# Kernel tuning notes

Hardware: AMD Instinct MI355X
Metric: run time of the kernel (lower is better)

The kernel has to match this reference:

```python
import jax, jax.numpy as jnp
import numpy as np

N = 1024
DH = 64   # XH feature dim (<= DOUT)
DP = 32   # XP feature dim
DIN = 64  # input_dim (== output_dim, required by f_psi applied to vij)
DOUT = 64 # output_dim
BN_EPS = 1e-5
SIGMA = 0.1


def setup_inputs() -> dict:
    key = jax.random.key(0)
    ks = jax.random.split(key, 8)
    return {
        "XH": jax.random.normal(ks[0], (N, DH), dtype=jnp.float32),
        "XP": jax.random.normal(ks[1], (N, DP), dtype=jnp.float32),
        "XX": jax.random.normal(ks[2], (N, DIN), dtype=jnp.float32),
        "K": 16,
        # nn.Parameter weight/bias: normal(0, 0.01)
        "weight": 0.01 * jax.random.normal(ks[3], (DIN, DOUT), dtype=jnp.float32),
        "bias": 0.01 * jax.random.normal(ks[4], (DOUT,), dtype=jnp.float32),
        # f_psi Linear params (torch kaiming-uniform ~ small uniform)
        "psi_w": jax.random.uniform(ks[5], (DOUT, DIN), dtype=jnp.float32, minval=-1.0, maxval=1.0) / np.sqrt(DIN),
        "psi_b": jax.random.uniform(ks[6], (DOUT,), dtype=jnp.float32, minval=-1.0, maxval=1.0) / np.sqrt(DIN),
        # BatchNorm1d affine params
        "gamma": jnp.ones((DOUT,), dtype=jnp.float32),
        "beta": jnp.zeros((DOUT,), dtype=jnp.float32),
    }


def _pairwise_norm(X):
    # [N, N] matrix of L2 norms of row differences (as in torch.norm(X[:,None]-X, dim=2))
    return jnp.linalg.norm(X[:, None, :] - X[None, :, :], axis=2)


def _adjacency(XH, XP, K, sigma=SIGMA):
    eps = float(np.finfo(np.float64).eps)
    XHs = XH / (sigma + eps)
    WHo = _pairwise_norm(XHs)
    WH = jnp.exp(-((WHo - WHo.min()) / (WHo.max() - WHo.min())) / 2)
    Wlo = _pairwise_norm(XP)
    Wl = jnp.exp(-((Wlo - Wlo.min()) / (Wlo.max() - Wlo.min())))
    WW = WH + 0.2 * Wl
    _, idx = jax.lax.top_k(WW, K)                       # per-row top-K neighbors
    n = WW.shape[0]
    mask = jnp.zeros_like(WW).at[jnp.arange(n)[:, None], idx].set(1.0)
    mask = mask + mask.T                                # symmetrize
    # Original sets Adj=WW/WW=1 where mask!=0 and Adj=WW-WW=0 elsewhere -> binary adjacency
    return (mask > 0).astype(WW.dtype)


def reference(XH, XP, XX, K, weight, bias, psi_w, psi_b, gamma, beta):
    Adj = _adjacency(XH, XP, K)                         # [N, N], {0,1}
    x = XX @ weight                                     # [N, D]
    vi = x[None, :, :] * Adj[:, :, None]                # [N, N, D]: vi[i,j] = x[j]*Adj[i,j]
    vij = x[None, :, :] + vi                            # [N, N, D]
    # f_psi: Linear -> BatchNorm1d (training-mode batch stats) -> Sigmoid, over N*N rows
    h = jnp.einsum('ijd,ed->ije', vij, psi_w) + psi_b   # [N, N, D]
    mu = h.mean(axis=(0, 1))                            # [D]
    var = h.var(axis=(0, 1))                            # biased var, as torch BN
    att = jax.nn.sigmoid((h - mu) * jax.lax.rsqrt(var + BN_EPS) * gamma + beta)
    # self-loop attention forced to 1 on the diagonal
    eye = jnp.eye(x.shape[0], dtype=bool)[:, :, None]
    att = jnp.where(eye, jnp.float32(1.0), att)
    out = (att * vi).sum(axis=0) + bias                 # [N, D]
    return (out[:, :XH.shape[1]], XP, out)
```

## Files before the change

### kernel.cpp

```cpp
#include <hip/hip_runtime.h>
#include <cfloat>

#define NN 1024


__global__ __launch_bounds__(256) void gcn_prep(const float* __restrict__ XH,
                                                const float* __restrict__ XP,
                                                const float* __restrict__ XX,
                                                const float* __restrict__ W,
                                                const float* __restrict__ psi_w,
                                                const int* __restrict__ kptr,
                                                float* __restrict__ XHT,
                                                float* __restrict__ XPT,
                                                float* __restrict__ x,
                                                float* __restrict__ y,
                                                double* __restrict__ Sbins,
                                                int* __restrict__ cdeg) {
    const int b = blockIdx.x;
    const int tid = threadIdx.x;
    __shared__ float th[64][65];
    __shared__ float tp[32][65];
    __shared__ float xybuf[4][2][64];
    if (b < 16) {
        const int j0 = b * 64;
#pragma unroll
        for (int it = 0; it < 16; ++it) {
            int idx = it * 256 + tid;
            int jl = idx >> 6, d = idx & 63;
            th[d][jl] = XH[(j0 + jl) * 64 + d];
        }
#pragma unroll
        for (int it = 0; it < 8; ++it) {
            int idx = it * 256 + tid;
            int jl = idx >> 5, d = idx & 31;
            tp[d][jl] = XP[(j0 + jl) * 32 + d];
        }
        __syncthreads();
#pragma unroll
        for (int it = 0; it < 16; ++it) {
            int idx = it * 256 + tid;
            int d = idx >> 6, jl = idx & 63;
            XHT[d * NN + j0 + jl] = th[d][jl];
        }
#pragma unroll
        for (int it = 0; it < 8; ++it) {
            int idx = it * 256 + tid;
            int d = idx >> 6, jl = idx & 63;
            XPT[d * NN + j0 + jl] = tp[d][jl];
        }
    } else if (b < 80) {
        const int w = tid >> 6, e = tid & 63;
        const int ibase = (b - 16) * 16 + w * 4;
#pragma unroll
        for (int r = 0; r < 4; ++r) {
            const int i = ibase + r;
            xybuf[w][0][e] = XX[i * 64 + e];
            __syncthreads();
            float acc = 0.f;
#pragma unroll
            for (int d = 0; d < 64; ++d) acc += xybuf[w][0][d] * W[d * 64 + e];
            x[i * 64 + e] = acc;
            xybuf[w][1][e] = acc;
            __syncthreads();
            float acc2 = 0.f;
            const float* pw = psi_w + e * 64;
#pragma unroll
            for (int d = 0; d < 64; ++d) acc2 += xybuf[w][1][d] * pw[d];
            y[i * 64 + e] = acc2;
        }
    } else {
        const int K = *kptr;
#pragma unroll
        for (int k = 0; k < 16; ++k) Sbins[tid * 16 + k] = 0.0;
#pragma unroll
        for (int q = 0; q < 4; ++q) cdeg[q * 256 + tid] = K;
    }
}

__global__ __launch_bounds__(256) void gcn_dist(const float* __restrict__ XH,
                                                const float* __restrict__ XP,
                                                const float* __restrict__ XHT,
                                                const float* __restrict__ XPT,
                                                float* __restrict__ dhp,
                                                float* __restrict__ dpp,
                                                float2* __restrict__ bmax) {
    const int b = blockIdx.x;
    const int i0 = (b >> 2) * 4;
    const int j = (b & 3) * 256 + threadIdx.x;
    const int tid = threadIdx.x;
    __shared__ float shi[4][64];
    __shared__ float spi[4][32];
    shi[tid >> 6][tid & 63] = XH[(i0 + (tid >> 6)) * 64 + (tid & 63)];
    if (tid < 128) spi[tid >> 5][tid & 31] = XP[(i0 + (tid >> 5)) * 32 + (tid & 31)];
    __syncthreads();
    float dh[4] = {0.f, 0.f, 0.f, 0.f}, dp[4] = {0.f, 0.f, 0.f, 0.f};
#pragma unroll 16
    for (int d = 0; d < 64; ++d) {
        float v = XHT[d * NN + j];
#pragma unroll
        for (int r = 0; r < 4; ++r) { float t = v - shi[r][d]; dh[r] += t * t; }
    }
#pragma unroll 16
    for (int d = 0; d < 32; ++d) {
        float v = XPT[d * NN + j];
#pragma unroll
        for (int r = 0; r < 4; ++r) { float t = v - spi[r][d]; dp[r] += t * t; }
    }
#pragma unroll
    for (int r = 0; r < 4; ++r) {
        dhp[(size_t)(i0 + r) * NN + j] = sqrtf(dh[r]);
        dpp[(size_t)(i0 + r) * NN + j] = sqrtf(dp[r]);
    }
    float mh = fmaxf(fmaxf(dh[0], dh[1]), fmaxf(dh[2], dh[3]));
    float mp = fmaxf(fmaxf(dp[0], dp[1]), fmaxf(dp[2], dp[3]));
#pragma unroll
    for (int m = 1; m < 64; m <<= 1) {
        mh = fmaxf(mh, __shfl_xor(mh, m));
        mp = fmaxf(mp, __shfl_xor(mp, m));
    }
    __shared__ float wmx[4][2];
    if ((tid & 63) == 0) { wmx[tid >> 6][0] = mh; wmx[tid >> 6][1] = mp; }
    __syncthreads();
    if (tid == 0) {
        float a = fmaxf(fmaxf(wmx[0][0], wmx[1][0]), fmaxf(wmx[2][0], wmx[3][0]));
        float b2 = fmaxf(fmaxf(wmx[0][1], wmx[1][1]), fmaxf(wmx[2][1], wmx[3][1]));
        bmax[b] = make_float2(a, b2);
    }
}

__global__ __launch_bounds__(256) void gcn_topk(const float* __restrict__ dhp,
                                                const float* __restrict__ dpp,
                                                const float2* __restrict__ bmax,
                                                const int* __restrict__ kptr,
                                                int* __restrict__ eidx,
                                                int* __restrict__ cdeg) {
    const int tid = threadIdx.x;
    const int w = tid >> 6, lane = tid & 63;
    const int i = blockIdx.x * 4 + w;
    float mh = 0.f, mp = 0.f;
#pragma unroll
    for (int q = 0; q < 4; ++q) {
        float2 v = bmax[q * 256 + tid];
        mh = fmaxf(mh, v.x); mp = fmaxf(mp, v.y);
    }
#pragma unroll
    for (int m = 1; m < 64; m <<= 1) {
        mh = fmaxf(mh, __shfl_xor(mh, m));
        mp = fmaxf(mp, __shfl_xor(mp, m));
    }
    __shared__ float warr[4][2];
    if (lane == 0) { warr[w][0] = mh; warr[w][1] = mp; }
    __syncthreads();
    mh = fmaxf(fmaxf(warr[0][0], warr[1][0]), fmaxf(warr[2][0], warr[3][0]));
    mp = fmaxf(fmaxf(warr[0][1], warr[1][1]), fmaxf(warr[2][1], warr[3][1]));
    const float cH = -0.5f / sqrtf(mh);
    const float cP = -1.0f / sqrtf(mp);
    const float4* dh4 = (const float4*)(dhp + (size_t)i * NN);
    const float4* dp4 = (const float4*)(dpp + (size_t)i * NN);
    unsigned long long kk[16];
#pragma unroll
    for (int s = 0; s < 4; ++s) {
        float4 a = dh4[s * 64 + lane];
        float4 b = dp4[s * 64 + lane];
        float w0 = __expf(a.x * cH) + 0.2f * __expf(b.x * cP);
        float w1 = __expf(a.y * cH) + 0.2f * __expf(b.y * cP);
        float w2 = __expf(a.z * cH) + 0.2f * __expf(b.z * cP);
        float w3 = __expf(a.w * cH) + 0.2f * __expf(b.w * cP);
        int jb = s * 256 + lane * 4;
        kk[s * 4 + 0] = ((unsigned long long)__float_as_uint(w0) << 32) | (unsigned)(1023 - (jb + 0));
        kk[s * 4 + 1] = ((unsigned long long)__float_as_uint(w1) << 32) | (unsigned)(1023 - (jb + 1));
        kk[s * 4 + 2] = ((unsigned long long)__float_as_uint(w2) << 32) | (unsigned)(1023 - (jb + 2));
        kk[s * 4 + 3] = ((unsigned long long)__float_as_uint(w3) << 32) | (unsigned)(1023 - (jb + 3));
    }
    const int K = *kptr;
    int jsave = 0;
    for (int t = 0; t < K; ++t) {
        unsigned long long bk = 0ull;
#pragma unroll
        for (int v = 0; v < 16; ++v) bk = kk[v] > bk ? kk[v] : bk;
#pragma unroll
        for (int m = 1; m < 64; m <<= 1) {
            unsigned long long o = __shfl_xor(bk, m);
            bk = o > bk ? o : bk;
        }
        int j = 1023 - (int)(bk & 0x3FFull);
        if (lane == t) jsave = j;
        if (((j >> 2) & 63) == lane) {
            int slot = ((j >> 8) << 2) | (j & 3);
#pragma unroll
            for (int v = 0; v < 16; ++v)
                if (v == slot) kk[v] = 0ull;
        }
    }
    if (lane < K) {
        eidx[i * 16 + lane] = jsave;
        atomicAdd(&cdeg[jsave], 1);
    }
}

__global__ __launch_bounds__(256) void gcn_overlap(const int* __restrict__ eidx,
                                                   int* __restrict__ cdeg) {
    const int gid = blockIdx.x * 256 + threadIdx.x;
    const int i = gid >> 4;
    const int j = eidx[gid];
    if (j < 0) return;
    const int4* ej = (const int4*)(eidx + j * 16);
    bool rec = false;
#pragma unroll
    for (int q = 0; q < 4; ++q) {
        int4 e = ej[q];
        rec |= (e.x == i) | (e.y == i) | (e.z == i) | (e.w == i);
    }
    if (rec) atomicSub(&cdeg[j], 1);
}

__global__ __launch_bounds__(256) void gcn_stats(const float* __restrict__ y,
                                                 const int* __restrict__ cdeg,
                                                 double* __restrict__ S1,
                                                 double* __restrict__ S2) {
    const int w = threadIdx.x >> 6, e = threadIdx.x & 63;
    const int j = blockIdx.x * 4 + w;
    const int c = cdeg[j];
    const double yd = (double)y[j * 64 + e];
    const int bin = (j & 31) * 64 + e;
    atomicAdd(&S1[bin], (double)(NN + c) * yd);
    atomicAdd(&S2[bin], (double)(NN + 3 * c) * yd * yd);
}

__global__ __launch_bounds__(256) void gcn_out(const float* __restrict__ x,
                                               const float* __restrict__ y,
                                               const int* __restrict__ cdeg,
                                               const float* __restrict__ gamma,
                                               const float* __restrict__ beta,
                                               const double* __restrict__ S1,
                                               const double* __restrict__ S2,
                                               const float* __restrict__ bias,
                                               const float* __restrict__ XP,
                                               float* __restrict__ out) {
    const int w = threadIdx.x >> 6, e = threadIdx.x & 63;
    const int j = blockIdx.x * 4 + w;
    double s1 = 0.0, s2 = 0.0;
#pragma unroll
    for (int b = 0; b < 32; ++b) { s1 += S1[b * 64 + e]; s2 += S2[b * 64 + e]; }
    const double m = s1 / 1048576.0;
    const double var = s2 / 1048576.0 - m * m;
    const float m0e = (float)m;
    const float scalee = (float)(1.0 / sqrt(var + 1e-5)) * gamma[e];
    float t = y[j * 64 + e];
    float z = (2.f * t - m0e) * scalee + beta[e];
    float s = 1.f / (1.f + expf(-z));
    float val = x[j * 64 + e] * ((float)(cdeg[j] - 1) * s + 1.f) + bias[e];
    out[j * 64 + e] = val;
    out[98304 + j * 64 + e] = val;
    if (e < 32) out[65536 + j * 32 + e] = XP[j * 32 + e];
}

extern "C" void kernel_launch(void* const* d_in, const int* in_sizes, int n_in,
                              void* d_out, int out_size, void* d_ws, size_t ws_size,
                              hipStream_t stream) {
    const float* XH    = (const float*)d_in[0];
    const float* XP    = (const float*)d_in[1];
    const float* XX    = (const float*)d_in[2];
    const int*   Kp    = (const int*)d_in[3];
    const float* W     = (const float*)d_in[4];
    const float* bias  = (const float*)d_in[5];
    const float* psi_w = (const float*)d_in[6];
    const float* psi_b = (const float*)d_in[7];
    const float* gamma = (const float*)d_in[8];
    const float* beta  = (const float*)d_in[9];
    (void)psi_b;
    float* out = (float*)d_out;
    char* ws = (char*)d_ws;

    float* dhp   = (float*)ws;
    float* dpp   = (float*)(ws + 0x400000);
    float* XHT   = (float*)(ws + 0x800000);
    float* XPT   = (float*)(ws + 0x840000);
    int* eidx    = (int*)(ws + 0x860000);
    float2* bmax = (float2*)(ws + 0x870000);
    int* cdeg    = (int*)(ws + 0x872000);
    double* S1   = (double*)(ws + 0x874000);
    double* S2   = (double*)(ws + 0x878000);
    float* x     = (float*)(ws + 0x880000);
    float* y     = (float*)(ws + 0x8C0000);

    gcn_prep<<<dim3(81), dim3(256), 0, stream>>>(XH, XP, XX, W, psi_w, Kp, XHT, XPT, x, y, S1, cdeg);
    gcn_dist<<<dim3(1024), dim3(256), 0, stream>>>(XH, XP, XHT, XPT, dhp, dpp, bmax);
    gcn_topk<<<dim3(256), dim3(256), 0, stream>>>(dhp, dpp, bmax, Kp, eidx, cdeg);
    gcn_overlap<<<dim3(64), dim3(256), 0, stream>>>(eidx, cdeg);
    gcn_stats<<<dim3(256), dim3(256), 0, stream>>>(y, cdeg, S1, S2);
    gcn_out<<<dim3(256), dim3(256), 0, stream>>>(x, y, cdeg, gamma, beta, S1, S2, bias, XP, out);
}
```

Measured before the change: 147.1 us.

## Fuse all stages into one cooperative kernel with grid-wide syncs

Replaces six separate kernel launches with a single cooperative launch of 256 blocks that uses grid.sync() between the prep, distance, top-k, overlap, stats and output stages. The distance stage is remapped so each block covers four rows across all 1024 columns instead of launching 1024 blocks. The aim is to remove per-launch overhead and inter-kernel gaps. In exchange, parallelism in the distance stage drops to 256 blocks, and each grid barrier has its own cost.

```diff
diff --git a/kernel.cpp b/kernel.cpp
--- a/kernel.cpp
+++ b/kernel.cpp
@@ -1,26 +1,37 @@
 #include <hip/hip_runtime.h>
+#include <hip/hip_cooperative_groups.h>
 #include <cfloat>
 
+namespace cg = cooperative_groups;
+
 #define NN 1024
 
 
-__global__ __launch_bounds__(256) void gcn_prep(const float* __restrict__ XH,
-                                                const float* __restrict__ XP,
-                                                const float* __restrict__ XX,
-                                                const float* __restrict__ W,
-                                                const float* __restrict__ psi_w,
-                                                const int* __restrict__ kptr,
-                                                float* __restrict__ XHT,
-                                                float* __restrict__ XPT,
-                                                float* __restrict__ x,
-                                                float* __restrict__ y,
-                                                double* __restrict__ Sbins,
-                                                int* __restrict__ cdeg) {
+__global__ __launch_bounds__(256, 1) void gcn_mega(
+    const float* __restrict__ XH, const float* __restrict__ XP,
+    const float* __restrict__ XX, const int* __restrict__ kptr,
+    const float* __restrict__ W, const float* __restrict__ bias,
+    const float* __restrict__ psi_w, const float* __restrict__ gamma,
+    const float* __restrict__ beta,
+    float* __restrict__ dhp, float* __restrict__ dpp,
+    float* __restrict__ XHT, float* __restrict__ XPT,
+    int* __restrict__ eidx, float2* __restrict__ bmax,
+    int* __restrict__ cdeg, double* __restrict__ S1, double* __restrict__ S2,
+    float* __restrict__ x, float* __restrict__ y,
+    float* __restrict__ out)
+{
+    cg::grid_group grid = cg::this_grid();
     const int b = blockIdx.x;
     const int tid = threadIdx.x;
+    const int w = tid >> 6, lane = tid & 63;
+
     __shared__ float th[64][65];
     __shared__ float tp[32][65];
     __shared__ float xybuf[4][2][64];
+    __shared__ float shi[4][64];
+    __shared__ float spi[4][32];
+    __shared__ float wred[4][2];
+
     if (b < 16) {
         const int j0 = b * 64;
 #pragma unroll
@@ -49,210 +60,182 @@
             XPT[d * NN + j0 + jl] = tp[d][jl];
         }
     } else if (b < 80) {
-        const int w = tid >> 6, e = tid & 63;
         const int ibase = (b - 16) * 16 + w * 4;
 #pragma unroll
         for (int r = 0; r < 4; ++r) {
             const int i = ibase + r;
-            xybuf[w][0][e] = XX[i * 64 + e];
+            xybuf[w][0][lane] = XX[i * 64 + lane];
             __syncthreads();
             float acc = 0.f;
 #pragma unroll
-            for (int d = 0; d < 64; ++d) acc += xybuf[w][0][d] * W[d * 64 + e];
-            x[i * 64 + e] = acc;
-            xybuf[w][1][e] = acc;
+            for (int d = 0; d < 64; ++d) acc += xybuf[w][0][d] * W[d * 64 + lane];
+            x[i * 64 + lane] = acc;
+            xybuf[w][1][lane] = acc;
             __syncthreads();
             float acc2 = 0.f;
-            const float* pw = psi_w + e * 64;
+            const float* pw = psi_w + lane * 64;
 #pragma unroll
             for (int d = 0; d < 64; ++d) acc2 += xybuf[w][1][d] * pw[d];
-            y[i * 64 + e] = acc2;
-        }
-    } else {
+            y[i * 64 + lane] = acc2;
+        }
+    } else if (b == 80) {
         const int K = *kptr;
 #pragma unroll
-        for (int k = 0; k < 16; ++k) Sbins[tid * 16 + k] = 0.0;
+        for (int k = 0; k < 16; ++k) S1[tid * 16 + k] = 0.0;
 #pragma unroll
         for (int q = 0; q < 4; ++q) cdeg[q * 256 + tid] = K;
     }
-}
-
-__global__ __launch_bounds__(256) void gcn_dist(const float* __restrict__ XH,
-                                                const float* __restrict__ XP,
-                                                const float* __restrict__ XHT,
-                                                const float* __restrict__ XPT,
-                                                float* __restrict__ dhp,
-                                                float* __restrict__ dpp,
-                                                float2* __restrict__ bmax) {
-    const int b = blockIdx.x;
-    const int i0 = (b >> 2) * 4;
-    const int j = (b & 3) * 256 + threadIdx.x;
-    const int tid = threadIdx.x;
-    __shared__ float shi[4][64];
-    __shared__ float spi[4][32];
-    shi[tid >> 6][tid & 63] = XH[(i0 + (tid >> 6)) * 64 + (tid & 63)];
-    if (tid < 128) spi[tid >> 5][tid & 31] = XP[(i0 + (tid >> 5)) * 32 + (tid & 31)];
-    __syncthreads();
-    float dh[4] = {0.f, 0.f, 0.f, 0.f}, dp[4] = {0.f, 0.f, 0.f, 0.f};
+    grid.sync();
+
+    {
+        const int i0 = b * 4;
+        shi[w][lane] = XH[(i0 + w) * 64 + lane];
+        if (tid < 128) spi[tid >> 5][tid & 31] = XP[(i0 + (tid >> 5)) * 32 + (tid & 31)];
+        __syncthreads();
+        float mh = 0.f, mp = 0.f;
+#pragma unroll
+        for (int jc = 0; jc < 4; ++jc) {
+            const int j = jc * 256 + tid;
+            float dh[4] = {0.f, 0.f, 0.f, 0.f}, dp[4] = {0.f, 0.f, 0.f, 0.f};
 #pragma unroll 16
-    for (int d = 0; d < 64; ++d) {
-        float v = XHT[d * NN + j];
-#pragma unroll
-        for (int r = 0; r < 4; ++r) { float t = v - shi[r][d]; dh[r] += t * t; }
-    }
+            for (int d = 0; d < 64; ++d) {
+                float v = XHT[d * NN + j];
+#pragma unroll
+                for (int r = 0; r < 4; ++r) { float t = v - shi[r][d]; dh[r] += t * t; }
+            }
 #pragma unroll 16
-    for (int d = 0; d < 32; ++d) {
-        float v = XPT[d * NN + j];
-#pragma unroll
-        for (int r = 0; r < 4; ++r) { float t = v - spi[r][d]; dp[r] += t * t; }
-    }
-#pragma unroll
-    for (int r = 0; r < 4; ++r) {
-        dhp[(size_t)(i0 + r) * NN + j] = sqrtf(dh[r]);
-        dpp[(size_t)(i0 + r) * NN + j] = sqrtf(dp[r]);
-    }
-    float mh = fmaxf(fmaxf(dh[0], dh[1]), fmaxf(dh[2], dh[3]));
-    float mp = fmaxf(fmaxf(dp[0], dp[1]), fmaxf(dp[2], dp[3]));
-#pragma unroll
-    for (int m = 1; m < 64; m <<= 1) {
-        mh = fmaxf(mh, __shfl_xor(mh, m));
-        mp = fmaxf(mp, __shfl_xor(mp, m));
-    }
-    __shared__ float wmx[4][2];
-    if ((tid & 63) == 0) { wmx[tid >> 6][0] = mh; wmx[tid >> 6][1] = mp; }
-    __syncthreads();
-    if (tid == 0) {
-        float a = fmaxf(fmaxf(wmx[0][0], wmx[1][0]), fmaxf(wmx[2][0], wmx[3][0]));
-        float b2 = fmaxf(fmaxf(wmx[0][1], wmx[1][1]), fmaxf(wmx[2][1], wmx[3][1]));
-        bmax[b] = make_float2(a, b2);
-    }
-}
-
-__global__ __launch_bounds__(256) void gcn_topk(const float* __restrict__ dhp,
-                                                const float* __restrict__ dpp,
-                                                const float2* __restrict__ bmax,
-                                                const int* __restrict__ kptr,
-                                                int* __restrict__ eidx,
-                                                int* __restrict__ cdeg) {
-    const int tid = threadIdx.x;
-    const int w = tid >> 6, lane = tid & 63;
-    const int i = blockIdx.x * 4 + w;
-    float mh = 0.f, mp = 0.f;
-#pragma unroll
-    for (int q = 0; q < 4; ++q) {
-        float2 v = bmax[q * 256 + tid];
-        mh = fmaxf(mh, v.x); mp = fmaxf(mp, v.y);
-    }
-#pragma unroll
-    for (int m = 1; m < 64; m <<= 1) {
-        mh = fmaxf(mh, __shfl_xor(mh, m));
-        mp = fmaxf(mp, __shfl_xor(mp, m));
-    }
-    __shared__ float warr[4][2];
-    if (lane == 0) { warr[w][0] = mh; warr[w][1] = mp; }
-    __syncthreads();
-    mh = fmaxf(fmaxf(warr[0][0], warr[1][0]), fmaxf(warr[2][0], warr[3][0]));
-    mp = fmaxf(fmaxf(warr[0][1], warr[1][1]), fmaxf(warr[2][1], warr[3][1]));
-    const float cH = -0.5f / sqrtf(mh);
-    const float cP = -1.0f / sqrtf(mp);
-    const float4* dh4 = (const float4*)(dhp + (size_t)i * NN);
-    const float4* dp4 = (const float4*)(dpp + (size_t)i * NN);
-    unsigned long long kk[16];
-#pragma unroll
-    for (int s = 0; s < 4; ++s) {
-        float4 a = dh4[s * 64 + lane];
-        float4 b = dp4[s * 64 + lane];
-        float w0 = __expf(a.x * cH) + 0.2f * __expf(b.x * cP);
-        float w1 = __expf(a.y * cH) + 0.2f * __expf(b.y * cP);
-        float w2 = __expf(a.z * cH) + 0.2f * __expf(b.z * cP);
-        float w3 = __expf(a.w * cH) + 0.2f * __expf(b.w * cP);
-        int jb = s * 256 + lane * 4;
-        kk[s * 4 + 0] = ((unsigned long long)__float_as_uint(w0) << 32) | (unsigned)(1023 - (jb + 0));
-        kk[s * 4 + 1] = ((unsigned long long)__float_as_uint(w1) << 32) | (unsigned)(1023 - (jb + 1));
-        kk[s * 4 + 2] = ((unsigned long long)__float_as_uint(w2) << 32) | (unsigned)(1023 - (jb + 2));
-        kk[s * 4 + 3] = ((unsigned long long)__float_as_uint(w3) << 32) | (unsigned)(1023 - (jb + 3));
-    }
-    const int K = *kptr;
-    int jsave = 0;
-    for (int t = 0; t < K; ++t) {
-        unsigned long long bk = 0ull;
-#pragma unroll
-        for (int v = 0; v < 16; ++v) bk = kk[v] > bk ? kk[v] : bk;
+            for (int d = 0; d < 32; ++d) {
+                float v = XPT[d * NN + j];
+#pragma unroll
+                for (int r = 0; r < 4; ++r) { float t = v - spi[r][d]; dp[r] += t * t; }
+            }
+#pragma unroll
+            for (int r = 0; r < 4; ++r) {
+                dhp[(size_t)(i0 + r) * NN + j] = sqrtf(dh[r]);
+                dpp[(size_t)(i0 + r) * NN + j] = sqrtf(dp[r]);
+            }
+            mh = fmaxf(mh, fmaxf(fmaxf(dh[0], dh[1]), fmaxf(dh[2], dh[3])));
+            mp = fmaxf(mp, fmaxf(fmaxf(dp[0], dp[1]), fmaxf(dp[2], dp[3])));
+        }
 #pragma unroll
         for (int m = 1; m < 64; m <<= 1) {
-            unsigned long long o = __shfl_xor(bk, m);
-            bk = o > bk ? o : bk;
-        }
-        int j = 1023 - (int)(bk & 0x3FFull);
-        if (lane == t) jsave = j;
-        if (((j >> 2) & 63) == lane) {
-            int slot = ((j >> 8) << 2) | (j & 3);
-#pragma unroll
-            for (int v = 0; v < 16; ++v)
-                if (v == slot) kk[v] = 0ull;
-        }
-    }
-    if (lane < K) {
-        eidx[i * 16 + lane] = jsave;
-        atomicAdd(&cdeg[jsave], 1);
-    }
-}
-
-__global__ __launch_bounds__(256) void gcn_overlap(const int* __restrict__ eidx,
-                                                   int* __restrict__ cdeg) {
-    const int gid = blockIdx.x * 256 + threadIdx.x;
-    const int i = gid >> 4;
-    const int j = eidx[gid];
-    if (j < 0) return;
-    const int4* ej = (const int4*)(eidx + j * 16);
-    bool rec = false;
-#pragma unroll
-    for (int q = 0; q < 4; ++q) {
-        int4 e = ej[q];
-        rec |= (e.x == i) | (e.y == i) | (e.z == i) | (e.w == i);
-    }
-    if (rec) atomicSub(&cdeg[j], 1);
-}
-
-__global__ __launch_bounds__(256) void gcn_stats(const float* __restrict__ y,
-                                                 const int* __restrict__ cdeg,
-                                                 double* __restrict__ S1,
-                                                 double* __restrict__ S2) {
-    const int w = threadIdx.x >> 6, e = threadIdx.x & 63;
-    const int j = blockIdx.x * 4 + w;
-    const int c = cdeg[j];
-    const double yd = (double)y[j * 64 + e];
-    const int bin = (j & 31) * 64 + e;
-    atomicAdd(&S1[bin], (double)(NN + c) * yd);
-    atomicAdd(&S2[bin], (double)(NN + 3 * c) * yd * yd);
-}
-
-__global__ __launch_bounds__(256) void gcn_out(const float* __restrict__ x,
-                                               const float* __restrict__ y,
-                                               const int* __restrict__ cdeg,
-                                               const float* __restrict__ gamma,
-                                               const float* __restrict__ beta,
-                                               const double* __restrict__ S1,
-                                               const double* __restrict__ S2,
-                                               const float* __restrict__ bias,
-                                               const float* __restrict__ XP,
-                                               float* __restrict__ out) {
-    const int w = threadIdx.x >> 6, e = threadIdx.x & 63;
-    const int j = blockIdx.x * 4 + w;
-    double s1 = 0.0, s2 = 0.0;
-#pragma unroll
-    for (int b = 0; b < 32; ++b) { s1 += S1[b * 64 + e]; s2 += S2[b * 64 + e]; }
-    const double m = s1 / 1048576.0;
-    const double var = s2 / 1048576.0 - m * m;
-    const float m0e = (float)m;
-    const float scalee = (float)(1.0 / sqrt(var + 1e-5)) * gamma[e];
-    float t = y[j * 64 + e];
-    float z = (2.f * t - m0e) * scalee + beta[e];
-    float s = 1.f / (1.f + expf(-z));
-    float val = x[j * 64 + e] * ((float)(cdeg[j] - 1) * s + 1.f) + bias[e];
-    out[j * 64 + e] = val;
-    out[98304 + j * 64 + e] = val;
-    if (e < 32) out[65536 + j * 32 + e] = XP[j * 32 + e];
+            mh = fmaxf(mh, __shfl_xor(mh, m));
+            mp = fmaxf(mp, __shfl_xor(mp, m));
+        }
+        if (lane == 0) { wred[w][0] = mh; wred[w][1] = mp; }
+        __syncthreads();
+        if (tid == 0) {
+            float a = fmaxf(fmaxf(wred[0][0], wred[1][0]), fmaxf(wred[2][0], wred[3][0]));
+            float b2 = fmaxf(fmaxf(wred[0][1], wred[1][1]), fmaxf(wred[2][1], wred[3][1]));
+            bmax[b] = make_float2(a, b2);
+        }
+    }
+    grid.sync();
+
+    {
+        float2 v = bmax[tid];
+        float mh = v.x, mp = v.y;
+#pragma unroll
+        for (int m = 1; m < 64; m <<= 1) {
+            mh = fmaxf(mh, __shfl_xor(mh, m));
+            mp = fmaxf(mp, __shfl_xor(mp, m));
+        }
+        __syncthreads();
+        if (lane == 0) { wred[w][0] = mh; wred[w][1] = mp; }
+        __syncthreads();
+        mh = fmaxf(fmaxf(wred[0][0], wred[1][0]), fmaxf(wred[2][0], wred[3][0]));
+        mp = fmaxf(fmaxf(wred[0][1], wred[1][1]), fmaxf(wred[2][1], wred[3][1]));
+        const float cH = -0.5f / sqrtf(mh);
+        const float cP = -1.0f / sqrtf(mp);
+        const int i = b * 4 + w;
+        const float4* dh4 = (const float4*)(dhp + (size_t)i * NN);
+        const float4* dp4 = (const float4*)(dpp + (size_t)i * NN);
+        unsigned long long kk[16];
+#pragma unroll
+        for (int s = 0; s < 4; ++s) {
+            float4 a = dh4[s * 64 + lane];
+            float4 bb = dp4[s * 64 + lane];
+            float w0 = __expf(a.x * cH) + 0.2f * __expf(bb.x * cP);
+            float w1 = __expf(a.y * cH) + 0.2f * __expf(bb.y * cP);
+            float w2 = __expf(a.z * cH) + 0.2f * __expf(bb.z * cP);
+            float w3 = __expf(a.w * cH) + 0.2f * __expf(bb.w * cP);
+            int jb = s * 256 + lane * 4;
+            kk[s * 4 + 0] = ((unsigned long long)__float_as_uint(w0) << 32) | (unsigned)(1023 - (jb + 0));
+            kk[s * 4 + 1] = ((unsigned long long)__float_as_uint(w1) << 32) | (unsigned)(1023 - (jb + 1));
+            kk[s * 4 + 2] = ((unsigned long long)__float_as_uint(w2) << 32) | (unsigned)(1023 - (jb + 2));
+            kk[s * 4 + 3] = ((unsigned long long)__float_as_uint(w3) << 32) | (unsigned)(1023 - (jb + 3));
+        }
+        const int K = *kptr;
+        int jsave = 0;
+        for (int t = 0; t < K; ++t) {
+            unsigned long long bk = 0ull;
+#pragma unroll
+            for (int vv = 0; vv < 16; ++vv) bk = kk[vv] > bk ? kk[vv] : bk;
+#pragma unroll
+            for (int m = 1; m < 64; m <<= 1) {
+                unsigned long long o = __shfl_xor(bk, m);
+                bk = o > bk ? o : bk;
+            }
+            int j = 1023 - (int)(bk & 0x3FFull);
+            if (lane == t) jsave = j;
+            if (((j >> 2) & 63) == lane) {
+                int slot = ((j >> 8) << 2) | (j & 3);
+#pragma unroll
+                for (int vv = 0; vv < 16; ++vv)
+                    if (vv == slot) kk[vv] = 0ull;
+            }
+        }
+        if (lane < K) {
+            eidx[i * 16 + lane] = jsave;
+            atomicAdd(&cdeg[jsave], 1);
+        }
+    }
+    grid.sync();
+
+    if (b < 64) {
+        const int gid = b * 256 + tid;
+        const int i = gid >> 4;
+        const int j = eidx[gid];
+        if (j >= 0) {
+            const int4* ej = (const int4*)(eidx + j * 16);
+            bool rec = false;
+#pragma unroll
+            for (int q = 0; q < 4; ++q) {
+                int4 e = ej[q];
+                rec |= (e.x == i) | (e.y == i) | (e.z == i) | (e.w == i);
+            }
+            if (rec) atomicSub(&cdeg[j], 1);
+        }
+    }
+    grid.sync();
+
+    {
+        const int j = b * 4 + w;
+        const int c = cdeg[j];
+        const double yd = (double)y[j * 64 + lane];
+        const int bin = (j & 31) * 64 + lane;
+        atomicAdd(&S1[bin], (double)(NN + c) * yd);
+        atomicAdd(&S2[bin], (double)(NN + 3 * c) * yd * yd);
+    }
+    grid.sync();
+
+    {
+        const int j = b * 4 + w;
+        double s1 = 0.0, s2 = 0.0;
+#pragma unroll
+        for (int q = 0; q < 32; ++q) { s1 += S1[q * 64 + lane]; s2 += S2[q * 64 + lane]; }
+        const double m = s1 / 1048576.0;
+        const double var = s2 / 1048576.0 - m * m;
+        const float m0e = (float)m;
+        const float scalee = (float)(1.0 / sqrt(var + 1e-5)) * gamma[lane];
+        float t = y[j * 64 + lane];
+        float z = (2.f * t - m0e) * scalee + beta[lane];
+        float s = 1.f / (1.f + expf(-z));
+        float val = x[j * 64 + lane] * ((float)(cdeg[j] - 1) * s + 1.f) + bias[lane];
+        out[j * 64 + lane] = val;
+        out[98304 + j * 64 + lane] = val;
+        if (lane < 32) out[65536 + j * 32 + lane] = XP[j * 32 + lane];
+    }
 }
 
 extern "C" void kernel_launch(void* const* d_in, const int* in_sizes, int n_in,
@@ -284,10 +267,13 @@
     float* x     = (float*)(ws + 0x880000);
     float* y     = (float*)(ws + 0x8C0000);
 
-    gcn_prep<<<dim3(81), dim3(256), 0, stream>>>(XH, XP, XX, W, psi_w, Kp, XHT, XPT, x, y, S1, cdeg);
-    gcn_dist<<<dim3(1024), dim3(256), 0, stream>>>(XH, XP, XHT, XPT, dhp, dpp, bmax);
-    gcn_topk<<<dim3(256), dim3(256), 0, stream>>>(dhp, dpp, bmax, Kp, eidx, cdeg);
-    gcn_overlap<<<dim3(64), dim3(256), 0, stream>>>(eidx, cdeg);
-    gcn_stats<<<dim3(256), dim3(256), 0, stream>>>(y, cdeg, S1, S2);
-    gcn_out<<<dim3(256), dim3(256), 0, stream>>>(x, y, cdeg, gamma, beta, S1, S2, bias, XP, out);
+    void* args[] = {
+        (void*)&XH, (void*)&XP, (void*)&XX, (void*)&Kp, (void*)&W, (void*)&bias,
+        (void*)&psi_w, (void*)&gamma, (void*)&beta,
+        (void*)&dhp, (void*)&dpp, (void*)&XHT, (void*)&XPT,
+        (void*)&eidx, (void*)&bmax, (void*)&cdeg, (void*)&S1, (void*)&S2,
+        (void*)&x, (void*)&y, (void*)&out
+    };
+    hipLaunchCooperativeKernel(reinterpret_cast<void*>(gcn_mega),
+                               dim3(256), dim3(256), args, 0, stream);
 }
```

Result: slower. 368.8 us (+150.7%).
